# Kernel optimization log

Hardware: AMD Instinct MI355X
Metric: run time of the kernel (lower is better)

Reference implementation:

```python
import jax, jax.numpy as jnp
import numpy as np

NU = 3
NUM_MEM_TOKENS = 128
EPS = 1e-5


def dpfp(x, nu=NU):
    # x: [..., d] -> [..., 2*nu*d]; all outputs are >= 0
    x = jnp.concatenate([jax.nn.relu(x), jax.nn.relu(-x)], axis=-1)
    x_rolled = jnp.concatenate([jnp.roll(x, shift=j, axis=-1) for j in range(1, nu + 1)], axis=-1)
    x_repeat = jnp.concatenate([x] * nu, axis=-1)
    return x_repeat * x_rolled


def setup_inputs() -> dict:
    key = jax.random.key(0)
    ks = jax.random.split(key, 8)
    B, S, D, DM = 1, 16384, 2048, 64
    DK = 2 * NU * DM  # 384
    scale = 0.02
    return {
        "hidden_states": jax.random.normal(ks[0], (B, S, D), jnp.float32),
        "Wmq": jax.random.normal(ks[1], (DM, D), jnp.float32) * scale,
        "Wmk": jax.random.normal(ks[2], (DM, D), jnp.float32) * scale,
        "Wmv": jax.random.normal(ks[3], (D, D), jnp.float32) * scale,
        "Wmb_w": jax.random.normal(ks[4], (1, D), jnp.float32) * scale,
        "Wmb_b": jax.random.normal(ks[5], (1,), jnp.float32),
        "W_mem": jax.random.normal(ks[6], (B, DK, D), jnp.float32) * scale,
        "z": jax.random.uniform(ks[7], (B, DK), jnp.float32) + 0.1,
    }


def reference(hidden_states, Wmq, Wmk, Wmv, Wmb_w, Wmb_b, W_mem, z):
    # ---- associate (read from fast-weight memory) ----
    mq = dpfp(hidden_states @ Wmq.T)                       # [b,s,dk]
    num = jnp.einsum('ijk,ikt->ijt', mq, W_mem)            # [b,s,d]
    denom = jnp.einsum('ik,ijk->ij', z, mq)[..., None] + EPS
    hidden_states = num / denom + hidden_states

    # wrapped transformer layer modeled as identity
    out = hidden_states

    # ---- update_mem (write: recurrent outer-product accumulation) ----
    mem_tokens = out[:, -NUM_MEM_TOKENS:]                  # [b,m,d]
    mk = dpfp(mem_tokens @ Wmk.T)                          # [b,m,dk]
    new_mv = mem_tokens @ Wmv.T                            # [b,m,d]

    num2 = jnp.einsum('ijk,ikt->ijt', mk, W_mem)           # [b,m,d]
    denom2 = jnp.einsum('ij,ikj->ik', z, mk)[..., None] + EPS
    prev_mv = num2 / denom2

    mk_sq = jnp.sum(mk * mk, axis=-1)                      # ||mk||^2, [b,m]
    new_info_coef = 1.0 - denom2 / (mk_sq + EPS)[..., None]
    new_info_coef = jax.lax.stop_gradient(jnp.clip(new_info_coef, 0.0, 1.0))

    mv = new_mv - prev_mv
    mb = jax.nn.sigmoid(mem_tokens @ Wmb_w.T + Wmb_b)[..., 0]  # [b,m]
    associations = jnp.einsum('ijk,ijt,ij->ikt', mk, mv, mb)   # [b,dk,d]

    W_mem_new = W_mem + associations
    z_new = z + jnp.sum(new_info_coef * mk, axis=1)
    return out, W_mem_new, z_new
```

## Files before the change

### kernel.cpp

```cpp
#include <hip/hip_runtime.h>
#include <hip/hip_bf16.h>
#include <math.h>

#define S_ 16384
#define D_ 2048
#define DM_ 64
#define DK_ 384
#define NMEM_ 128
#define EPS_ 1e-5f

typedef __attribute__((ext_vector_type(8))) short bf16x8;
typedef __attribute__((ext_vector_type(8))) short s16x8;
typedef __attribute__((ext_vector_type(4))) float f32x4;
typedef unsigned short u16;

static __device__ __forceinline__ u16 f2bf(float x) {
    __hip_bfloat16 h = __float2bfloat16(x);
    return *reinterpret_cast<u16*>(&h);
}

static __device__ __forceinline__ void gload16(const void* g, void* l) {
    __builtin_amdgcn_global_load_lds(
        (const __attribute__((address_space(1))) unsigned int*)g,
        (__attribute__((address_space(3))) unsigned int*)l, 16, 0, 0);
}

__global__ __launch_bounds__(256) void k_prep(const float* __restrict__ Wmq,
                                              const float* __restrict__ Wmv,
                                              const float* __restrict__ Wmem,
                                              u16* __restrict__ Wmq_b,
                                              u16* __restrict__ Wmv_b,
                                              u16* __restrict__ WmT) {
    __shared__ float ts[32][33];
    const int bid = blockIdx.x;
    const int tid = threadIdx.x;
    if (bid < 4096) {
        size_t idx = ((size_t)bid * 256 + tid) * 4;
        float4 v = *reinterpret_cast<const float4*>(&Wmv[idx]);
        ushort4 p;
        p.x = f2bf(v.x); p.y = f2bf(v.y); p.z = f2bf(v.z); p.w = f2bf(v.w);
        *reinterpret_cast<ushort4*>(&Wmv_b[idx]) = p;
    } else if (bid < 4224) {
        int idx = ((bid - 4096) * 256 + tid) * 4;
        float4 v = *reinterpret_cast<const float4*>(&Wmq[idx]);
        ushort4 p;
        p.x = f2bf(v.x); p.y = f2bf(v.y); p.z = f2bf(v.z); p.w = f2bf(v.w);
        *reinterpret_cast<ushort4*>(&Wmq_b[idx]) = p;
    } else {
        int t = bid - 4224;
        int c0 = (t & 63) * 32, k0 = (t >> 6) * 32;
        const int tx = tid & 31, ty = tid >> 5;
#pragma unroll
        for (int i = 0; i < 4; ++i)
            ts[ty + 8 * i][tx] = Wmem[(size_t)(k0 + ty + 8 * i) * D_ + c0 + tx];
        __syncthreads();
#pragma unroll
        for (int i = 0; i < 4; ++i)
            WmT[(size_t)(c0 + ty + 8 * i) * DK_ + k0 + tx] = f2bf(ts[tx][ty + 8 * i]);
    }
}

__global__ __launch_bounds__(256) void k_qdp(const float* __restrict__ hs,
                                             const u16* __restrict__ Wmq_b,
                                             const float* __restrict__ z,
                                             u16* __restrict__ mq_b,
                                             float* __restrict__ denomv) {
    __shared__ u16 As[32 * 64];
    __shared__ u16 Bs[64 * 64];
    __shared__ float xs[32][128];
    __shared__ float zs[DK_];
    const int r0 = blockIdx.x * 32;
    const int tid = threadIdx.x;
    const int lane = tid & 63, w = tid >> 6;
    const int lrow = lane & 15, lkg = lane >> 4;
    const int wr = w >> 1, wc = w & 1;
    for (int i = tid; i < DK_; i += 256) zs[i] = z[i];
    f32x4 acc[2];
    const f32x4 zero4 = {0.f, 0.f, 0.f, 0.f};
    acc[0] = zero4; acc[1] = zero4;
    for (int kc = 0; kc < D_ / 64; ++kc) {
#pragma unroll
        for (int i = 0; i < 2; ++i) {
            int flat4 = tid + 256 * i;
            int row = flat4 >> 4, c4 = flat4 & 15;
            const float4 v = *reinterpret_cast<const float4*>(
                &hs[(size_t)(r0 + row) * D_ + kc * 64 + c4 * 4]);
            int off = row * 64 + (((c4 >> 1) ^ (row & 7)) * 8) + (c4 & 1) * 4;
            ushort4 p;
            p.x = f2bf(v.x); p.y = f2bf(v.y); p.z = f2bf(v.z); p.w = f2bf(v.w);
            *reinterpret_cast<ushort4*>(&As[off]) = p;
        }
#pragma unroll
        for (int i = 0; i < 2; ++i) {
            int col = w * 16 + i * 8 + (lane >> 3);
            int gg = (lane & 7) ^ (col & 7);
            gload16(Wmq_b + (size_t)col * D_ + kc * 64 + gg * 8,
                    &Bs[(w * 16 + i * 8) * 64]);
        }
        __syncthreads();
#pragma unroll
        for (int s = 0; s < 2; ++s) {
            int rl = wr * 16 + lrow;
            bf16x8 a_ = *reinterpret_cast<const bf16x8*>(
                &As[rl * 64 + (((s * 4 + lkg) ^ (rl & 7)) * 8)]);
#pragma unroll
            for (int n = 0; n < 2; ++n) {
                int cl = wc * 32 + n * 16 + lrow;
                bf16x8 b_ = *reinterpret_cast<const bf16x8*>(
                    &Bs[cl * 64 + (((s * 4 + lkg) ^ (cl & 7)) * 8)]);
                acc[n] = __builtin_amdgcn_mfma_f32_16x16x32_bf16(a_, b_, acc[n], 0, 0, 0);
            }
        }
        __syncthreads();
    }
#pragma unroll
    for (int n = 0; n < 2; ++n) {
        int col = wc * 32 + n * 16 + lrow;
#pragma unroll
        for (int r = 0; r < 4; ++r) {
            int row = wr * 16 + lkg * 4 + r;
            float q = acc[n][r];
            xs[row][col] = fmaxf(q, 0.f);
            xs[row][col + 64] = fmaxf(-q, 0.f);
        }
    }
    __syncthreads();
    {
        int row = tid >> 3, sub = tid & 7;
        float pd = 0.f;
#pragma unroll
        for (int c = 0; c < 6; ++c) {
            int base = sub * 48 + c * 8;
            int g = base >> 7;
            s16x8 pk;
#pragma unroll
            for (int e = 0; e < 8; ++e) {
                int m = base + e;
                int i = m & 127;
                float v = xs[row][i] * xs[row][(i - g - 1) & 127];
                pd += zs[m] * v;
                pk[e] = (short)f2bf(v);
            }
            *reinterpret_cast<s16x8*>(&mq_b[(size_t)(r0 + row) * DK_ + base]) = pk;
        }
        pd += __shfl_down(pd, 4, 8);
        pd += __shfl_down(pd, 2, 8);
        pd += __shfl_down(pd, 1, 8);
        if (sub == 0) denomv[r0 + row] = pd + EPS_;
    }
}

__global__ __launch_bounds__(256) void k_main(const float* __restrict__ hs,
                                              const u16* __restrict__ mq_b,
                                              const u16* __restrict__ WmT,
                                              const float* __restrict__ denomv,
                                              float* __restrict__ out) {
    __shared__ u16 At[128 * 64];
    __shared__ u16 Bt[128 * 64];
    __shared__ float dinv[128];
    const int bid = blockIdx.x;
    const int swz = (bid & 7) * 256 + (bid >> 3);
    const int r0 = (swz >> 4) * 128, c0 = (swz & 15) * 128;
    const int tid = threadIdx.x;
    const int lane = tid & 63, w = tid >> 6;
    const int lrow = lane & 15, lkg = lane >> 4;
    const int wr = w >> 1, wc = w & 1;
    if (tid < 128) dinv[tid] = 1.f / denomv[r0 + tid];
    f32x4 acc[4][4];
    const f32x4 zero4 = {0.f, 0.f, 0.f, 0.f};
#pragma unroll
    for (int m = 0; m < 4; ++m)
#pragma unroll
        for (int n = 0; n < 4; ++n) acc[m][n] = zero4;
    for (int kc = 0; kc < 6; ++kc) {
#pragma unroll
        for (int i = 0; i < 4; ++i) {
            int rr = w * 32 + i * 8 + (lane >> 3);
            int gg = (lane & 7) ^ (rr & 7);
            gload16(mq_b + (size_t)(r0 + rr) * DK_ + kc * 64 + gg * 8,
                    &At[(w * 32 + i * 8) * 64]);
            gload16(WmT + (size_t)(c0 + rr) * DK_ + kc * 64 + gg * 8,
                    &Bt[(w * 32 + i * 8) * 64]);
        }
        __syncthreads();
#pragma unroll
        for (int s = 0; s < 2; ++s) {
            bf16x8 af[4], bb[4];
#pragma unroll
            for (int m = 0; m < 4; ++m) {
                int rl = wr * 64 + m * 16 + lrow;
                af[m] = *reinterpret_cast<const bf16x8*>(
                    &At[rl * 64 + (((s * 4 + lkg) ^ (rl & 7)) * 8)]);
            }
#pragma unroll
            for (int n = 0; n < 4; ++n) {
                int cl = wc * 64 + n * 16 + lrow;
                bb[n] = *reinterpret_cast<const bf16x8*>(
                    &Bt[cl * 64 + (((s * 4 + lkg) ^ (cl & 7)) * 8)]);
            }
#pragma unroll
            for (int m = 0; m < 4; ++m)
#pragma unroll
                for (int n = 0; n < 4; ++n)
                    acc[m][n] = __builtin_amdgcn_mfma_f32_16x16x32_bf16(
                        af[m], bb[n], acc[m][n], 0, 0, 0);
        }
        __syncthreads();
    }
#pragma unroll
    for (int m = 0; m < 4; ++m)
#pragma unroll
        for (int n = 0; n < 4; ++n) {
            int colg = c0 + wc * 64 + n * 16 + lrow;
#pragma unroll
            for (int r = 0; r < 4; ++r) {
                int rowl = wr * 64 + m * 16 + lkg * 4 + r;
                size_t off = (size_t)(r0 + rowl) * D_ + colg;
                out[off] = acc[m][n][r] * dinv[rowl] + hs[off];
            }
        }
}

__global__ __launch_bounds__(256) void k_mk(const float* __restrict__ out,
                                            const float* __restrict__ Wmk,
                                            const float* __restrict__ Wmb_w,
                                            const float* __restrict__ Wmb_b,
                                            const float* __restrict__ z,
                                            float* __restrict__ mk_g,
                                            u16* __restrict__ mk_b,
                                            u16* __restrict__ mem_b,
                                            float* __restrict__ scal) {
    __shared__ float memRow[D_];
    __shared__ float qpart[4][64];
    __shared__ float xv[128];
    __shared__ float mks[DK_];
    __shared__ float red[256];
    const int j = blockIdx.x;
    const int tid = threadIdx.x;
    const float* mem = out + (size_t)(S_ - NMEM_ + j) * D_;
    const float4* mem4 = reinterpret_cast<const float4*>(mem);
    float4* mr4 = reinterpret_cast<float4*>(memRow);
#pragma unroll
    for (int i4 = tid; i4 < 512; i4 += 256) {
        float4 v = mem4[i4];
        mr4[i4] = v;
        ushort4 p;
        p.x = f2bf(v.x); p.y = f2bf(v.y); p.z = f2bf(v.z); p.w = f2bf(v.w);
        *reinterpret_cast<ushort4*>(&mem_b[(size_t)j * D_ + i4 * 4]) = p;
    }
    __syncthreads();
    {
        int c = tid & 63, seg = tid >> 6;
        const float4* wrow = reinterpret_cast<const float4*>(Wmk + (size_t)c * D_);
        float p = 0.f;
#pragma unroll 4
        for (int k4 = seg * 128; k4 < seg * 128 + 128; ++k4) {
            float4 a = mr4[k4], b = wrow[k4];
            p += a.x * b.x + a.y * b.y + a.z * b.z + a.w * b.w;
        }
        qpart[seg][c] = p;
    }
    __syncthreads();
    if (tid < 64) {
        float q = qpart[0][tid] + qpart[1][tid] + qpart[2][tid] + qpart[3][tid];
        xv[tid] = fmaxf(q, 0.f);
        xv[tid + 64] = fmaxf(-q, 0.f);
    }
    __syncthreads();
    for (int m = tid; m < DK_; m += 256) {
        int i = m & 127, g = m >> 7;
        float v = xv[i] * xv[(i - g - 1) & 127];
        mks[m] = v;
        mk_g[(size_t)j * DK_ + m] = v;
        mk_b[(size_t)j * DK_ + m] = f2bf(v);
    }
    __syncthreads();
    float pd = 0.f, ps = 0.f;
    for (int m = tid; m < DK_; m += 256) { float v = mks[m]; pd += v * z[m]; ps += v * v; }
    red[tid] = pd; __syncthreads();
    for (int s = 128; s > 0; s >>= 1) { if (tid < s) red[tid] += red[tid + s]; __syncthreads(); }
    float denom2 = red[0] + EPS_;
    __syncthreads();
    red[tid] = ps; __syncthreads();
    for (int s = 128; s > 0; s >>= 1) { if (tid < s) red[tid] += red[tid + s]; __syncthreads(); }
    float mksq = red[0];
    __syncthreads();
    float pb = 0.f;
    {
        const float4* wb4 = reinterpret_cast<const float4*>(Wmb_w);
#pragma unroll
        for (int k4 = tid; k4 < 512; k4 += 256) {
            float4 a = mr4[k4], b = wb4[k4];
            pb += a.x * b.x + a.y * b.y + a.z * b.z + a.w * b.w;
        }
    }
    red[tid] = pb; __syncthreads();
    for (int s = 128; s > 0; s >>= 1) { if (tid < s) red[tid] += red[tid + s]; __syncthreads(); }
    if (tid == 0) {
        float bsum = red[0] + Wmb_b[0];
        float mb = 1.f / (1.f + expf(-bsum));
        float nic = 1.f - denom2 / (mksq + EPS_);
        nic = fminf(fmaxf(nic, 0.f), 1.f);
        scal[j * 4 + 0] = denom2;
        scal[j * 4 + 1] = nic;
        scal[j * 4 + 2] = mb;
        scal[j * 4 + 3] = mksq;
    }
}

__global__ __launch_bounds__(256) void k_mv(const u16* __restrict__ mem_b,
                                            const u16* __restrict__ Wmv_b,
                                            const u16* __restrict__ mk_b,
                                            const u16* __restrict__ WmT,
                                            const float* __restrict__ scal,
                                            float* __restrict__ mvb) {
    __shared__ u16 At[128 * 64];
    __shared__ u16 Bt[64 * 64];
    __shared__ float inv2[128];
    __shared__ float mbl[128];
    const int c0 = blockIdx.x * 64;
    const int tid = threadIdx.x;
    const int lane = tid & 63, w = tid >> 6;
    const int lrow = lane & 15, lkg = lane >> 4;
    const int wr = w >> 1, wc = w & 1;
    if (tid < 128) {
        inv2[tid] = 1.f / scal[tid * 4 + 0];
        mbl[tid] = scal[tid * 4 + 2];
    }
    f32x4 acc1[4][2], acc2[4][2];
    const f32x4 zero4 = {0.f, 0.f, 0.f, 0.f};
#pragma unroll
    for (int m = 0; m < 4; ++m)
#pragma unroll
        for (int n = 0; n < 2; ++n) { acc1[m][n] = zero4; acc2[m][n] = zero4; }
    for (int kc = 0; kc < D_ / 64; ++kc) {
#pragma unroll
        for (int i = 0; i < 4; ++i) {
            int rr = w * 32 + i * 8 + (lane >> 3);
            int gg = (lane & 7) ^ (rr & 7);
            gload16(mem_b + (size_t)rr * D_ + kc * 64 + gg * 8,
                    &At[(w * 32 + i * 8) * 64]);
        }
#pragma unroll
        for (int i = 0; i < 2; ++i) {
            int cc = w * 16 + i * 8 + (lane >> 3);
            int gg = (lane & 7) ^ (cc & 7);
            gload16(Wmv_b + (size_t)(c0 + cc) * D_ + kc * 64 + gg * 8,
                    &Bt[(w * 16 + i * 8) * 64]);
        }
        __syncthreads();
#pragma unroll
        for (int s = 0; s < 2; ++s) {
            bf16x8 af[4], bb[2];
#pragma unroll
            for (int m = 0; m < 4; ++m) {
                int rl = wr * 64 + m * 16 + lrow;
                af[m] = *reinterpret_cast<const bf16x8*>(
                    &At[rl * 64 + (((s * 4 + lkg) ^ (rl & 7)) * 8)]);
            }
#pragma unroll
            for (int n = 0; n < 2; ++n) {
                int cl = wc * 32 + n * 16 + lrow;
                bb[n] = *reinterpret_cast<const bf16x8*>(
                    &Bt[cl * 64 + (((s * 4 + lkg) ^ (cl & 7)) * 8)]);
            }
#pragma unroll
            for (int m = 0; m < 4; ++m)
#pragma unroll
                for (int n = 0; n < 2; ++n)
                    acc1[m][n] = __builtin_amdgcn_mfma_f32_16x16x32_bf16(
                        af[m], bb[n], acc1[m][n], 0, 0, 0);
        }
        __syncthreads();
    }
    for (int kc = 0; kc < 6; ++kc) {
#pragma unroll
        for (int i = 0; i < 4; ++i) {
            int rr = w * 32 + i * 8 + (lane >> 3);
            int gg = (lane & 7) ^ (rr & 7);
            gload16(mk_b + (size_t)rr * DK_ + kc * 64 + gg * 8,
                    &At[(w * 32 + i * 8) * 64]);
        }
#pragma unroll
        for (int i = 0; i < 2; ++i) {
            int cc = w * 16 + i * 8 + (lane >> 3);
            int gg = (lane & 7) ^ (cc & 7);
            gload16(WmT + (size_t)(c0 + cc) * DK_ + kc * 64 + gg * 8,
                    &Bt[(w * 16 + i * 8) * 64]);
        }
        __syncthreads();
#pragma unroll
        for (int s = 0; s < 2; ++s) {
            bf16x8 af[4], bb[2];
#pragma unroll
            for (int m = 0; m < 4; ++m) {
                int rl = wr * 64 + m * 16 + lrow;
                af[m] = *reinterpret_cast<const bf16x8*>(
                    &At[rl * 64 + (((s * 4 + lkg) ^ (rl & 7)) * 8)]);
            }
#pragma unroll
            for (int n = 0; n < 2; ++n) {
                int cl = wc * 32 + n * 16 + lrow;
                bb[n] = *reinterpret_cast<const bf16x8*>(
                    &Bt[cl * 64 + (((s * 4 + lkg) ^ (cl & 7)) * 8)]);
            }
#pragma unroll
            for (int m = 0; m < 4; ++m)
#pragma unroll
                for (int n = 0; n < 2; ++n)
                    acc2[m][n] = __builtin_amdgcn_mfma_f32_16x16x32_bf16(
                        af[m], bb[n], acc2[m][n], 0, 0, 0);
        }
        __syncthreads();
    }
#pragma unroll
    for (int m = 0; m < 4; ++m)
#pragma unroll
        for (int n = 0; n < 2; ++n) {
            int colg = c0 + wc * 32 + n * 16 + lrow;
#pragma unroll
            for (int r = 0; r < 4; ++r) {
                int j = wr * 64 + m * 16 + lkg * 4 + r;
                mvb[(size_t)j * D_ + colg] =
                    (acc1[m][n][r] - acc2[m][n][r] * inv2[j]) * mbl[j];
            }
        }
}

__global__ __launch_bounds__(256) void k_wmem(const float* __restrict__ Wmem,
                                              const float* __restrict__ mk_g,
                                              const float* __restrict__ mvb,
                                              const float* __restrict__ scal,
                                              const float* __restrict__ z,
                                              float* __restrict__ wout,
                                              float* __restrict__ zout) {
    const int tid = threadIdx.x;
    if (blockIdx.y == 48) {
        if (blockIdx.x == 0) {
            for (int t = tid; t < DK_; t += 256) {
                float acc = z[t];
                for (int j = 0; j < NMEM_; ++j)
                    acc += scal[j * 4 + 1] * mk_g[(size_t)j * DK_ + t];
                zout[t] = acc;
            }
        }
        return;
    }
    const int c0 = blockIdx.x * 256;
    const int k0 = blockIdx.y * 8;
    const int tk = tid >> 5, tt = tid & 31;
    const float4* mvb4 = reinterpret_cast<const float4*>(mvb);
    f32x4 acc[2] = {{0.f, 0.f, 0.f, 0.f}, {0.f, 0.f, 0.f, 0.f}};
#pragma unroll 4
    for (int j = 0; j < NMEM_; ++j) {
        float a = mk_g[(size_t)j * DK_ + k0 + tk];
#pragma unroll
        for (int i = 0; i < 2; ++i) {
            float4 v = mvb4[((size_t)j * D_ + c0 + tt * 4 + 128 * i) >> 2];
            acc[i][0] += a * v.x; acc[i][1] += a * v.y;
            acc[i][2] += a * v.z; acc[i][3] += a * v.w;
        }
    }
#pragma unroll
    for (int i = 0; i < 2; ++i) {
        size_t off = (size_t)(k0 + tk) * D_ + c0 + tt * 4 + 128 * i;
        float4 wv = *reinterpret_cast<const float4*>(&Wmem[off]);
        float4 o;
        o.x = wv.x + acc[i][0]; o.y = wv.y + acc[i][1];
        o.z = wv.z + acc[i][2]; o.w = wv.w + acc[i][3];
        *reinterpret_cast<float4*>(&wout[off]) = o;
    }
}

extern "C" void kernel_launch(void* const* d_in, const int* in_sizes, int n_in,
                              void* d_out, int out_size, void* d_ws, size_t ws_size,
                              hipStream_t stream) {
    const float* hs   = (const float*)d_in[0];
    const float* Wmq  = (const float*)d_in[1];
    const float* Wmk  = (const float*)d_in[2];
    const float* Wmv  = (const float*)d_in[3];
    const float* Wmbw = (const float*)d_in[4];
    const float* Wmbb = (const float*)d_in[5];
    const float* Wmem = (const float*)d_in[6];
    const float* z    = (const float*)d_in[7];
    float* out  = (float*)d_out;
    float* wout = out + (size_t)S_ * D_;
    float* zout = wout + (size_t)DK_ * D_;

    float* ws = (float*)d_ws;
    float* denomv = ws;
    float* mk_g   = denomv + S_;
    float* scal   = mk_g + (size_t)NMEM_ * DK_;
    float* mvb    = scal + NMEM_ * 4;
    u16* mq_b  = (u16*)(mvb + (size_t)NMEM_ * D_);
    u16* WmT   = mq_b + (size_t)S_ * DK_;
    u16* Wmq_b = WmT + (size_t)D_ * DK_;
    u16* Wmv_b = Wmq_b + (size_t)DM_ * D_;
    u16* mem_b = Wmv_b + (size_t)D_ * D_;
    u16* mk_b  = mem_b + (size_t)NMEM_ * D_;

    k_prep<<<dim3(4992), 256, 0, stream>>>(Wmq, Wmv, Wmem, Wmq_b, Wmv_b, WmT);
    k_qdp<<<dim3(S_ / 32), 256, 0, stream>>>(hs, Wmq_b, z, mq_b, denomv);
    k_main<<<dim3((S_ / 128) * (D_ / 128)), 256, 0, stream>>>(hs, mq_b, WmT, denomv, out);
    k_mk<<<dim3(NMEM_), 256, 0, stream>>>(out, Wmk, Wmbw, Wmbb, z, mk_g, mk_b, mem_b, scal);
    k_mv<<<dim3(D_ / 64), 256, 0, stream>>>(mem_b, Wmv_b, mk_b, WmT, scal, mvb);
    k_wmem<<<dim3(D_ / 256, DK_ / 8 + 1), 256, 0, stream>>>(Wmem, mk_g, mvb, scal, z, wout, zout);
}
```

Measured before the change: 198.2 us.

## Fuse DPFP query projection with memory readout GEMM in one kernel

Merges k_qdp and k_main into a single kernel. Each 32-row block computes the query projection, builds the DPFP features as bf16 A-fragments held in registers, then sweeps all 2048 output columns against WmT staged in shared memory. This removes the global round trip of mq_b and denomv and one launch. The cost is a much smaller row tile (32 rows instead of 128), so WmT (about 1.5 MB in bf16) is reloaded by each of 512 blocks. The DPFP inputs are also now rounded to bf16 before the products are taken.

```diff
diff --git a/kernel.cpp b/kernel.cpp
--- a/kernel.cpp
+++ b/kernel.cpp
@@ -17,6 +17,11 @@
 static __device__ __forceinline__ u16 f2bf(float x) {
     __hip_bfloat16 h = __float2bfloat16(x);
     return *reinterpret_cast<u16*>(&h);
+}
+
+static __device__ __forceinline__ float bf2f(u16 u) {
+    union { unsigned int i; float f; } c; c.i = ((unsigned int)u) << 16;
+    return c.f;
 }
 
 static __device__ __forceinline__ void gload16(const void* g, void* l) {
@@ -60,24 +65,26 @@
     }
 }
 
-__global__ __launch_bounds__(256) void k_qdp(const float* __restrict__ hs,
-                                             const u16* __restrict__ Wmq_b,
-                                             const float* __restrict__ z,
-                                             u16* __restrict__ mq_b,
-                                             float* __restrict__ denomv) {
-    __shared__ u16 As[32 * 64];
-    __shared__ u16 Bs[64 * 64];
-    __shared__ float xs[32][128];
+__global__ __launch_bounds__(256) void k_fuse(const float* __restrict__ hs,
+                                              const u16* __restrict__ Wmq_b,
+                                              const u16* __restrict__ WmT,
+                                              const float* __restrict__ z,
+                                              float* __restrict__ out) {
+    __shared__ u16 sbuf[16384];
     __shared__ float zs[DK_];
+    __shared__ float dinvS[32];
     const int r0 = blockIdx.x * 32;
     const int tid = threadIdx.x;
     const int lane = tid & 63, w = tid >> 6;
     const int lrow = lane & 15, lkg = lane >> 4;
     const int wr = w >> 1, wc = w & 1;
     for (int i = tid; i < DK_; i += 256) zs[i] = z[i];
-    f32x4 acc[2];
+
+    u16* As = sbuf;
+    u16* Bs = sbuf + 2048;
+    f32x4 q1[2];
     const f32x4 zero4 = {0.f, 0.f, 0.f, 0.f};
-    acc[0] = zero4; acc[1] = zero4;
+    q1[0] = zero4; q1[1] = zero4;
     for (int kc = 0; kc < D_ / 64; ++kc) {
 #pragma unroll
         for (int i = 0; i < 2; ++i) {
@@ -108,117 +115,90 @@
                 int cl = wc * 32 + n * 16 + lrow;
                 bf16x8 b_ = *reinterpret_cast<const bf16x8*>(
                     &Bs[cl * 64 + (((s * 4 + lkg) ^ (cl & 7)) * 8)]);
-                acc[n] = __builtin_amdgcn_mfma_f32_16x16x32_bf16(a_, b_, acc[n], 0, 0, 0);
-            }
-        }
-        __syncthreads();
-    }
+                q1[n] = __builtin_amdgcn_mfma_f32_16x16x32_bf16(a_, b_, q1[n], 0, 0, 0);
+            }
+        }
+        __syncthreads();
+    }
+
+    u16* xs = sbuf;
 #pragma unroll
     for (int n = 0; n < 2; ++n) {
         int col = wc * 32 + n * 16 + lrow;
 #pragma unroll
         for (int r = 0; r < 4; ++r) {
             int row = wr * 16 + lkg * 4 + r;
-            float q = acc[n][r];
-            xs[row][col] = fmaxf(q, 0.f);
-            xs[row][col + 64] = fmaxf(-q, 0.f);
-        }
-    }
-    __syncthreads();
+            float qv = q1[n][r];
+            xs[row * 136 + col] = f2bf(fmaxf(qv, 0.f));
+            xs[row * 136 + col + 64] = f2bf(fmaxf(-qv, 0.f));
+        }
+    }
+    __syncthreads();
+
+    bf16x8 af[12];
+    float pd = 0.f;
     {
-        int row = tid >> 3, sub = tid & 7;
-        float pd = 0.f;
-#pragma unroll
-        for (int c = 0; c < 6; ++c) {
-            int base = sub * 48 + c * 8;
-            int g = base >> 7;
-            s16x8 pk;
+        int arow = wr * 16 + lrow;
+#pragma unroll
+        for (int f = 0; f < 12; ++f) {
+            bf16x8 pk;
 #pragma unroll
             for (int e = 0; e < 8; ++e) {
-                int m = base + e;
-                int i = m & 127;
-                float v = xs[row][i] * xs[row][(i - g - 1) & 127];
+                int m = f * 32 + lkg * 8 + e;
+                int g = m >> 7, i = m & 127;
+                float v = bf2f(xs[arow * 136 + i]) *
+                          bf2f(xs[arow * 136 + ((i - g - 1) & 127)]);
                 pd += zs[m] * v;
                 pk[e] = (short)f2bf(v);
             }
-            *reinterpret_cast<s16x8*>(&mq_b[(size_t)(r0 + row) * DK_ + base]) = pk;
-        }
-        pd += __shfl_down(pd, 4, 8);
-        pd += __shfl_down(pd, 2, 8);
-        pd += __shfl_down(pd, 1, 8);
-        if (sub == 0) denomv[r0 + row] = pd + EPS_;
-    }
-}
-
-__global__ __launch_bounds__(256) void k_main(const float* __restrict__ hs,
-                                              const u16* __restrict__ mq_b,
-                                              const u16* __restrict__ WmT,
-                                              const float* __restrict__ denomv,
-                                              float* __restrict__ out) {
-    __shared__ u16 At[128 * 64];
-    __shared__ u16 Bt[128 * 64];
-    __shared__ float dinv[128];
-    const int bid = blockIdx.x;
-    const int swz = (bid & 7) * 256 + (bid >> 3);
-    const int r0 = (swz >> 4) * 128, c0 = (swz & 15) * 128;
-    const int tid = threadIdx.x;
-    const int lane = tid & 63, w = tid >> 6;
-    const int lrow = lane & 15, lkg = lane >> 4;
-    const int wr = w >> 1, wc = w & 1;
-    if (tid < 128) dinv[tid] = 1.f / denomv[r0 + tid];
-    f32x4 acc[4][4];
-    const f32x4 zero4 = {0.f, 0.f, 0.f, 0.f};
-#pragma unroll
-    for (int m = 0; m < 4; ++m)
-#pragma unroll
-        for (int n = 0; n < 4; ++n) acc[m][n] = zero4;
-    for (int kc = 0; kc < 6; ++kc) {
-#pragma unroll
-        for (int i = 0; i < 4; ++i) {
-            int rr = w * 32 + i * 8 + (lane >> 3);
-            int gg = (lane & 7) ^ (rr & 7);
-            gload16(mq_b + (size_t)(r0 + rr) * DK_ + kc * 64 + gg * 8,
-                    &At[(w * 32 + i * 8) * 64]);
-            gload16(WmT + (size_t)(c0 + rr) * DK_ + kc * 64 + gg * 8,
-                    &Bt[(w * 32 + i * 8) * 64]);
-        }
-        __syncthreads();
-#pragma unroll
-        for (int s = 0; s < 2; ++s) {
-            bf16x8 af[4], bb[4];
-#pragma unroll
-            for (int m = 0; m < 4; ++m) {
-                int rl = wr * 64 + m * 16 + lrow;
-                af[m] = *reinterpret_cast<const bf16x8*>(
-                    &At[rl * 64 + (((s * 4 + lkg) ^ (rl & 7)) * 8)]);
-            }
-#pragma unroll
-            for (int n = 0; n < 4; ++n) {
-                int cl = wc * 64 + n * 16 + lrow;
-                bb[n] = *reinterpret_cast<const bf16x8*>(
-                    &Bt[cl * 64 + (((s * 4 + lkg) ^ (cl & 7)) * 8)]);
-            }
-#pragma unroll
-            for (int m = 0; m < 4; ++m)
-#pragma unroll
-                for (int n = 0; n < 4; ++n)
-                    acc[m][n] = __builtin_amdgcn_mfma_f32_16x16x32_bf16(
-                        af[m], bb[n], acc[m][n], 0, 0, 0);
-        }
-        __syncthreads();
-    }
-#pragma unroll
-    for (int m = 0; m < 4; ++m)
+            af[f] = pk;
+        }
+        pd += __shfl_xor(pd, 16);
+        pd += __shfl_xor(pd, 32);
+        if (wc == 0 && lane < 16) dinvS[wr * 16 + lane] = 1.f / (pd + EPS_);
+    }
+    __syncthreads();
+
+    f32x4 acc[4];
+#pragma unroll
+    for (int n = 0; n < 4; ++n) acc[n] = zero4;
+    for (int ct = 0; ct < 16; ++ct) {
+        const int c0 = ct * 128;
+        for (int kc = 0; kc < 3; ++kc) {
+#pragma unroll
+            for (int i = 0; i < 8; ++i) {
+                int flat = w * 64 + (lane) + 256 * i;
+                int cc = flat >> 4, g4 = flat & 15;
+                int gswz = g4 ^ (cc & 7);
+                gload16(WmT + (size_t)(c0 + cc) * DK_ + kc * 128 + gswz * 8,
+                        &sbuf[(w * 64 + 256 * i) * 8]);
+            }
+            __syncthreads();
+#pragma unroll
+            for (int s = 0; s < 4; ++s) {
+#pragma unroll
+                for (int n = 0; n < 4; ++n) {
+                    int cl = wc * 64 + n * 16 + lrow;
+                    bf16x8 bb = *reinterpret_cast<const bf16x8*>(
+                        &sbuf[cl * 128 + (((s * 4 + lkg) ^ (cl & 7)) * 8)]);
+                    acc[n] = __builtin_amdgcn_mfma_f32_16x16x32_bf16(
+                        af[kc * 4 + s], bb, acc[n], 0, 0, 0);
+                }
+            }
+            __syncthreads();
+        }
 #pragma unroll
         for (int n = 0; n < 4; ++n) {
             int colg = c0 + wc * 64 + n * 16 + lrow;
 #pragma unroll
             for (int r = 0; r < 4; ++r) {
-                int rowl = wr * 64 + m * 16 + lkg * 4 + r;
+                int rowl = wr * 16 + lkg * 4 + r;
                 size_t off = (size_t)(r0 + rowl) * D_ + colg;
-                out[off] = acc[m][n][r] * dinv[rowl] + hs[off];
-            }
-        }
+                out[off] = acc[n][r] * dinvS[rowl] + hs[off];
+            }
+            acc[n] = zero4;
+        }
+    }
 }
 
 __global__ __launch_bounds__(256) void k_mk(const float* __restrict__ out,
@@ -488,20 +468,17 @@
     float* zout = wout + (size_t)DK_ * D_;
 
     float* ws = (float*)d_ws;
-    float* denomv = ws;
-    float* mk_g   = denomv + S_;
+    float* mk_g   = ws;
     float* scal   = mk_g + (size_t)NMEM_ * DK_;
     float* mvb    = scal + NMEM_ * 4;
-    u16* mq_b  = (u16*)(mvb + (size_t)NMEM_ * D_);
-    u16* WmT   = mq_b + (size_t)S_ * DK_;
+    u16* WmT   = (u16*)(mvb + (size_t)NMEM_ * D_);
     u16* Wmq_b = WmT + (size_t)D_ * DK_;
     u16* Wmv_b = Wmq_b + (size_t)DM_ * D_;
     u16* mem_b = Wmv_b + (size_t)D_ * D_;
     u16* mk_b  = mem_b + (size_t)NMEM_ * D_;
 
     k_prep<<<dim3(4992), 256, 0, stream>>>(Wmq, Wmv, Wmem, Wmq_b, Wmv_b, WmT);
-    k_qdp<<<dim3(S_ / 32), 256, 0, stream>>>(hs, Wmq_b, z, mq_b, denomv);
-    k_main<<<dim3((S_ / 128) * (D_ / 128)), 256, 0, stream>>>(hs, mq_b, WmT, denomv, out);
+    k_fuse<<<dim3(S_ / 32), 256, 0, stream>>>(hs, Wmq_b, WmT, z, out);
     k_mk<<<dim3(NMEM_), 256, 0, stream>>>(out, Wmk, Wmbw, Wmbb, z, mk_g, mk_b, mem_b, scal);
     k_mv<<<dim3(D_ / 64), 256, 0, stream>>>(mem_b, Wmv_b, mk_b, WmT, scal, mvb);
     k_wmem<<<dim3(D_ / 256, DK_ / 8 + 1), 256, 0, stream>>>(Wmem, mk_g, mvb, scal, z, wout, zout);
```

Measured after the change: 236.2 us. +19.1%, slower.

## Double-buffer k_qdp K-loop and stage k_main epilogue through LDS for coalesced stores

Applied to the files above, without the earlier changes.

k_qdp now double-buffers its A and B tiles, issuing the next chunk's global loads before the MFMAs on the current chunk and converting and storing them afterwards. This drops one barrier per iteration and overlaps load latency with compute. k_main's epilogue now stages the scaled accumulator through LDS in two 64-row halves, then does coalesced float4 reads of hs and float4 writes of out. This replaces the scattered scalar stores, at the cost of extra LDS traffic and barriers.

```diff
diff --git a/kernel.cpp b/kernel.cpp
--- a/kernel.cpp
+++ b/kernel.cpp
@@ -65,10 +65,9 @@
                                              const float* __restrict__ z,
                                              u16* __restrict__ mq_b,
                                              float* __restrict__ denomv) {
-    __shared__ u16 As[32 * 64];
-    __shared__ u16 Bs[64 * 64];
-    __shared__ float xs[32][128];
+    __shared__ __align__(16) u16 qbuf[12288];
     __shared__ float zs[DK_];
+    float* xs = reinterpret_cast<float*>(qbuf);
     const int r0 = blockIdx.x * 32;
     const int tid = threadIdx.x;
     const int lane = tid & 63, w = tid >> 6;
@@ -78,40 +77,70 @@
     f32x4 acc[2];
     const f32x4 zero4 = {0.f, 0.f, 0.f, 0.f};
     acc[0] = zero4; acc[1] = zero4;
-    for (int kc = 0; kc < D_ / 64; ++kc) {
-#pragma unroll
-        for (int i = 0; i < 2; ++i) {
-            int flat4 = tid + 256 * i;
-            int row = flat4 >> 4, c4 = flat4 & 15;
-            const float4 v = *reinterpret_cast<const float4*>(
-                &hs[(size_t)(r0 + row) * D_ + kc * 64 + c4 * 4]);
-            int off = row * 64 + (((c4 >> 1) ^ (row & 7)) * 8) + (c4 & 1) * 4;
-            ushort4 p;
-            p.x = f2bf(v.x); p.y = f2bf(v.y); p.z = f2bf(v.z); p.w = f2bf(v.w);
-            *reinterpret_cast<ushort4*>(&As[off]) = p;
-        }
+    const int arow0 = tid >> 4, ac4_0 = tid & 15;
+    const int arow1 = (tid + 256) >> 4, ac4_1 = (tid + 256) & 15;
+    const int aoff0 = arow0 * 64 + (((ac4_0 >> 1) ^ (arow0 & 7)) * 8) + (ac4_0 & 1) * 4;
+    const int aoff1 = arow1 * 64 + (((ac4_1 >> 1) ^ (arow1 & 7)) * 8) + (ac4_1 & 1) * 4;
+    {
+        float4 v0 = *reinterpret_cast<const float4*>(&hs[(size_t)(r0 + arow0) * D_ + ac4_0 * 4]);
+        float4 v1 = *reinterpret_cast<const float4*>(&hs[(size_t)(r0 + arow1) * D_ + ac4_1 * 4]);
+        ushort4 p0, p1;
+        p0.x = f2bf(v0.x); p0.y = f2bf(v0.y); p0.z = f2bf(v0.z); p0.w = f2bf(v0.w);
+        p1.x = f2bf(v1.x); p1.y = f2bf(v1.y); p1.z = f2bf(v1.z); p1.w = f2bf(v1.w);
+        *reinterpret_cast<ushort4*>(&qbuf[aoff0]) = p0;
+        *reinterpret_cast<ushort4*>(&qbuf[aoff1]) = p1;
 #pragma unroll
         for (int i = 0; i < 2; ++i) {
             int col = w * 16 + i * 8 + (lane >> 3);
             int gg = (lane & 7) ^ (col & 7);
-            gload16(Wmq_b + (size_t)col * D_ + kc * 64 + gg * 8,
-                    &Bs[(w * 16 + i * 8) * 64]);
-        }
-        __syncthreads();
+            gload16(Wmq_b + (size_t)col * D_ + gg * 8, &qbuf[4096 + (w * 16 + i * 8) * 64]);
+        }
+    }
+    __syncthreads();
+    int cur = 0;
+    for (int kc = 0; kc < 32; ++kc) {
+        const int nxt = cur ^ 1;
+        const bool hasN = (kc + 1) < 32;
+        u16* Acur = qbuf + cur * 2048;
+        u16* Anxt = qbuf + nxt * 2048;
+        u16* Bcur = qbuf + 4096 + cur * 4096;
+        u16* Bnxt = qbuf + 4096 + nxt * 4096;
+        float4 v0, v1;
+        if (hasN) {
+            v0 = *reinterpret_cast<const float4*>(
+                &hs[(size_t)(r0 + arow0) * D_ + (kc + 1) * 64 + ac4_0 * 4]);
+            v1 = *reinterpret_cast<const float4*>(
+                &hs[(size_t)(r0 + arow1) * D_ + (kc + 1) * 64 + ac4_1 * 4]);
+#pragma unroll
+            for (int i = 0; i < 2; ++i) {
+                int col = w * 16 + i * 8 + (lane >> 3);
+                int gg = (lane & 7) ^ (col & 7);
+                gload16(Wmq_b + (size_t)col * D_ + (kc + 1) * 64 + gg * 8,
+                        &Bnxt[(w * 16 + i * 8) * 64]);
+            }
+        }
 #pragma unroll
         for (int s = 0; s < 2; ++s) {
             int rl = wr * 16 + lrow;
             bf16x8 a_ = *reinterpret_cast<const bf16x8*>(
-                &As[rl * 64 + (((s * 4 + lkg) ^ (rl & 7)) * 8)]);
+                &Acur[rl * 64 + (((s * 4 + lkg) ^ (rl & 7)) * 8)]);
 #pragma unroll
             for (int n = 0; n < 2; ++n) {
                 int cl = wc * 32 + n * 16 + lrow;
                 bf16x8 b_ = *reinterpret_cast<const bf16x8*>(
-                    &Bs[cl * 64 + (((s * 4 + lkg) ^ (cl & 7)) * 8)]);
+                    &Bcur[cl * 64 + (((s * 4 + lkg) ^ (cl & 7)) * 8)]);
                 acc[n] = __builtin_amdgcn_mfma_f32_16x16x32_bf16(a_, b_, acc[n], 0, 0, 0);
             }
         }
-        __syncthreads();
+        if (hasN) {
+            ushort4 p0, p1;
+            p0.x = f2bf(v0.x); p0.y = f2bf(v0.y); p0.z = f2bf(v0.z); p0.w = f2bf(v0.w);
+            p1.x = f2bf(v1.x); p1.y = f2bf(v1.y); p1.z = f2bf(v1.z); p1.w = f2bf(v1.w);
+            *reinterpret_cast<ushort4*>(&Anxt[aoff0]) = p0;
+            *reinterpret_cast<ushort4*>(&Anxt[aoff1]) = p1;
+        }
+        __syncthreads();
+        cur ^= 1;
     }
 #pragma unroll
     for (int n = 0; n < 2; ++n) {
@@ -120,8 +149,8 @@
         for (int r = 0; r < 4; ++r) {
             int row = wr * 16 + lkg * 4 + r;
             float q = acc[n][r];
-            xs[row][col] = fmaxf(q, 0.f);
-            xs[row][col + 64] = fmaxf(-q, 0.f);
+            xs[row * 128 + col] = fmaxf(q, 0.f);
+            xs[row * 128 + col + 64] = fmaxf(-q, 0.f);
         }
     }
     __syncthreads();
@@ -137,7 +166,7 @@
             for (int e = 0; e < 8; ++e) {
                 int m = base + e;
                 int i = m & 127;
-                float v = xs[row][i] * xs[row][(i - g - 1) & 127];
+                float v = xs[row * 128 + i] * xs[row * 128 + ((i - g - 1) & 127)];
                 pd += zs[m] * v;
                 pk[e] = (short)f2bf(v);
             }
@@ -155,9 +184,10 @@
                                               const u16* __restrict__ WmT,
                                               const float* __restrict__ denomv,
                                               float* __restrict__ out) {
-    __shared__ u16 At[128 * 64];
-    __shared__ u16 Bt[128 * 64];
+    __shared__ __align__(16) u16 ldsbuf[16384];
     __shared__ float dinv[128];
+    u16* At = ldsbuf;
+    u16* Bt = ldsbuf + 8192;
     const int bid = blockIdx.x;
     const int swz = (bid & 7) * 256 + (bid >> 3);
     const int r0 = (swz >> 4) * 128, c0 = (swz & 15) * 128;
@@ -207,18 +237,36 @@
         }
         __syncthreads();
     }
-#pragma unroll
-    for (int m = 0; m < 4; ++m)
-#pragma unroll
-        for (int n = 0; n < 4; ++n) {
-            int colg = c0 + wc * 64 + n * 16 + lrow;
-#pragma unroll
-            for (int r = 0; r < 4; ++r) {
-                int rowl = wr * 64 + m * 16 + lkg * 4 + r;
-                size_t off = (size_t)(r0 + rowl) * D_ + colg;
-                out[off] = acc[m][n][r] * dinv[rowl] + hs[off];
-            }
-        }
+    float* ldsf = reinterpret_cast<float*>(ldsbuf);
+    float4* ldsf4 = reinterpret_cast<float4*>(ldsbuf);
+#pragma unroll
+    for (int h = 0; h < 2; ++h) {
+        if (wr == h) {
+#pragma unroll
+            for (int m = 0; m < 4; ++m)
+#pragma unroll
+                for (int n = 0; n < 4; ++n) {
+                    int col = wc * 64 + n * 16 + lrow;
+#pragma unroll
+                    for (int r = 0; r < 4; ++r) {
+                        int rowl = m * 16 + lkg * 4 + r;
+                        ldsf[rowl * 128 + col] = acc[m][n][r] * dinv[h * 64 + rowl];
+                    }
+                }
+        }
+        __syncthreads();
+#pragma unroll
+        for (int i = 0; i < 8; ++i) {
+            int idx4 = tid + 256 * i;
+            int rowl = idx4 >> 5, c4 = idx4 & 31;
+            float4 v = ldsf4[idx4];
+            size_t off = (size_t)(r0 + h * 64 + rowl) * D_ + c0 + c4 * 4;
+            const float4 hv = *reinterpret_cast<const float4*>(&hs[off]);
+            v.x += hv.x; v.y += hv.y; v.z += hv.z; v.w += hv.w;
+            *reinterpret_cast<float4*>(&out[off]) = v;
+        }
+        __syncthreads();
+    }
 }
 
 __global__ __launch_bounds__(256) void k_mk(const float* __restrict__ out,
```

Result: no change. 202.1 us (+2.0%).

## Fuse bf16 conversion of Wmv/mem into k_mv, retile k_qdp, coalesce k_main epilogue

Applied to the files above, without the earlier changes.

Drops the separate fp32-to-bf16 conversion of Wmv (a 2048x2048 matrix) and of the memory tokens. k_mv now reads fp32 directly and converts while staging into LDS, which removes a large prep write/read pass. k_qdp moves to 16-row tiles with one MFMA per wave, doubling the block count for better occupancy and sharing one LDS buffer between phases. k_main's epilogue is staged through LDS so the output stores and hs reads become coalesced float4 accesses, at the cost of extra barriers.

```diff
diff --git a/kernel.cpp b/kernel.cpp
--- a/kernel.cpp
+++ b/kernel.cpp
@@ -26,28 +26,20 @@
 }
 
 __global__ __launch_bounds__(256) void k_prep(const float* __restrict__ Wmq,
-                                              const float* __restrict__ Wmv,
                                               const float* __restrict__ Wmem,
                                               u16* __restrict__ Wmq_b,
-                                              u16* __restrict__ Wmv_b,
                                               u16* __restrict__ WmT) {
     __shared__ float ts[32][33];
     const int bid = blockIdx.x;
     const int tid = threadIdx.x;
-    if (bid < 4096) {
-        size_t idx = ((size_t)bid * 256 + tid) * 4;
-        float4 v = *reinterpret_cast<const float4*>(&Wmv[idx]);
-        ushort4 p;
-        p.x = f2bf(v.x); p.y = f2bf(v.y); p.z = f2bf(v.z); p.w = f2bf(v.w);
-        *reinterpret_cast<ushort4*>(&Wmv_b[idx]) = p;
-    } else if (bid < 4224) {
-        int idx = ((bid - 4096) * 256 + tid) * 4;
+    if (bid < 128) {
+        int idx = (bid * 256 + tid) * 4;
         float4 v = *reinterpret_cast<const float4*>(&Wmq[idx]);
         ushort4 p;
         p.x = f2bf(v.x); p.y = f2bf(v.y); p.z = f2bf(v.z); p.w = f2bf(v.w);
         *reinterpret_cast<ushort4*>(&Wmq_b[idx]) = p;
     } else {
-        int t = bid - 4224;
+        int t = bid - 128;
         int c0 = (t & 63) * 32, k0 = (t >> 6) * 32;
         const int tx = tid & 31, ty = tid >> 5;
 #pragma unroll
@@ -65,30 +57,26 @@
                                              const float* __restrict__ z,
                                              u16* __restrict__ mq_b,
                                              float* __restrict__ denomv) {
-    __shared__ u16 As[32 * 64];
-    __shared__ u16 Bs[64 * 64];
-    __shared__ float xs[32][128];
+    __shared__ __align__(16) u16 qbuf[5376];
     __shared__ float zs[DK_];
-    const int r0 = blockIdx.x * 32;
+    u16* As = qbuf;
+    u16* Bs = qbuf + 1024;
+    float* xs = reinterpret_cast<float*>(qbuf);
+    const int r0 = blockIdx.x * 16;
     const int tid = threadIdx.x;
     const int lane = tid & 63, w = tid >> 6;
     const int lrow = lane & 15, lkg = lane >> 4;
-    const int wr = w >> 1, wc = w & 1;
     for (int i = tid; i < DK_; i += 256) zs[i] = z[i];
-    f32x4 acc[2];
-    const f32x4 zero4 = {0.f, 0.f, 0.f, 0.f};
-    acc[0] = zero4; acc[1] = zero4;
-    for (int kc = 0; kc < D_ / 64; ++kc) {
-#pragma unroll
-        for (int i = 0; i < 2; ++i) {
-            int flat4 = tid + 256 * i;
-            int row = flat4 >> 4, c4 = flat4 & 15;
+    f32x4 acc = {0.f, 0.f, 0.f, 0.f};
+    const int arow = tid >> 4, ac4 = tid & 15;
+    const int aoff = arow * 64 + (((ac4 >> 1) ^ (arow & 7)) * 8) + (ac4 & 1) * 4;
+    for (int kc = 0; kc < 32; ++kc) {
+        {
             const float4 v = *reinterpret_cast<const float4*>(
-                &hs[(size_t)(r0 + row) * D_ + kc * 64 + c4 * 4]);
-            int off = row * 64 + (((c4 >> 1) ^ (row & 7)) * 8) + (c4 & 1) * 4;
+                &hs[(size_t)(r0 + arow) * D_ + kc * 64 + ac4 * 4]);
             ushort4 p;
             p.x = f2bf(v.x); p.y = f2bf(v.y); p.z = f2bf(v.z); p.w = f2bf(v.w);
-            *reinterpret_cast<ushort4*>(&As[off]) = p;
+            *reinterpret_cast<ushort4*>(&As[aoff]) = p;
         }
 #pragma unroll
         for (int i = 0; i < 2; ++i) {
@@ -100,52 +88,48 @@
         __syncthreads();
 #pragma unroll
         for (int s = 0; s < 2; ++s) {
-            int rl = wr * 16 + lrow;
             bf16x8 a_ = *reinterpret_cast<const bf16x8*>(
-                &As[rl * 64 + (((s * 4 + lkg) ^ (rl & 7)) * 8)]);
-#pragma unroll
-            for (int n = 0; n < 2; ++n) {
-                int cl = wc * 32 + n * 16 + lrow;
-                bf16x8 b_ = *reinterpret_cast<const bf16x8*>(
-                    &Bs[cl * 64 + (((s * 4 + lkg) ^ (cl & 7)) * 8)]);
-                acc[n] = __builtin_amdgcn_mfma_f32_16x16x32_bf16(a_, b_, acc[n], 0, 0, 0);
-            }
-        }
-        __syncthreads();
-    }
-#pragma unroll
-    for (int n = 0; n < 2; ++n) {
-        int col = wc * 32 + n * 16 + lrow;
+                &As[lrow * 64 + (((s * 4 + lkg) ^ (lrow & 7)) * 8)]);
+            int cl = w * 16 + lrow;
+            bf16x8 b_ = *reinterpret_cast<const bf16x8*>(
+                &Bs[cl * 64 + (((s * 4 + lkg) ^ (cl & 7)) * 8)]);
+            acc = __builtin_amdgcn_mfma_f32_16x16x32_bf16(a_, b_, acc, 0, 0, 0);
+        }
+        __syncthreads();
+    }
+    {
+        int col = w * 16 + lrow;
 #pragma unroll
         for (int r = 0; r < 4; ++r) {
-            int row = wr * 16 + lkg * 4 + r;
-            float q = acc[n][r];
-            xs[row][col] = fmaxf(q, 0.f);
-            xs[row][col + 64] = fmaxf(-q, 0.f);
+            int row = lkg * 4 + r;
+            float q = acc[r];
+            xs[row * 132 + col] = fmaxf(q, 0.f);
+            xs[row * 132 + col + 64] = fmaxf(-q, 0.f);
         }
     }
     __syncthreads();
     {
-        int row = tid >> 3, sub = tid & 7;
+        int row = tid >> 4, sub = tid & 15;
         float pd = 0.f;
 #pragma unroll
-        for (int c = 0; c < 6; ++c) {
-            int base = sub * 48 + c * 8;
+        for (int c = 0; c < 3; ++c) {
+            int base = sub * 24 + c * 8;
             int g = base >> 7;
             s16x8 pk;
 #pragma unroll
             for (int e = 0; e < 8; ++e) {
                 int m = base + e;
                 int i = m & 127;
-                float v = xs[row][i] * xs[row][(i - g - 1) & 127];
+                float v = xs[row * 132 + i] * xs[row * 132 + ((i - g - 1) & 127)];
                 pd += zs[m] * v;
                 pk[e] = (short)f2bf(v);
             }
             *reinterpret_cast<s16x8*>(&mq_b[(size_t)(r0 + row) * DK_ + base]) = pk;
         }
-        pd += __shfl_down(pd, 4, 8);
-        pd += __shfl_down(pd, 2, 8);
-        pd += __shfl_down(pd, 1, 8);
+        pd += __shfl_down(pd, 8, 16);
+        pd += __shfl_down(pd, 4, 16);
+        pd += __shfl_down(pd, 2, 16);
+        pd += __shfl_down(pd, 1, 16);
         if (sub == 0) denomv[r0 + row] = pd + EPS_;
     }
 }
@@ -155,9 +139,10 @@
                                               const u16* __restrict__ WmT,
                                               const float* __restrict__ denomv,
                                               float* __restrict__ out) {
-    __shared__ u16 At[128 * 64];
-    __shared__ u16 Bt[128 * 64];
+    __shared__ __align__(16) u16 ldsbuf[16384];
     __shared__ float dinv[128];
+    u16* At = ldsbuf;
+    u16* Bt = ldsbuf + 8192;
     const int bid = blockIdx.x;
     const int swz = (bid & 7) * 256 + (bid >> 3);
     const int r0 = (swz >> 4) * 128, c0 = (swz & 15) * 128;
@@ -207,18 +192,36 @@
         }
         __syncthreads();
     }
-#pragma unroll
-    for (int m = 0; m < 4; ++m)
-#pragma unroll
-        for (int n = 0; n < 4; ++n) {
-            int colg = c0 + wc * 64 + n * 16 + lrow;
-#pragma unroll
-            for (int r = 0; r < 4; ++r) {
-                int rowl = wr * 64 + m * 16 + lkg * 4 + r;
-                size_t off = (size_t)(r0 + rowl) * D_ + colg;
-                out[off] = acc[m][n][r] * dinv[rowl] + hs[off];
-            }
-        }
+    float* ldsf = reinterpret_cast<float*>(ldsbuf);
+    float4* ldsf4 = reinterpret_cast<float4*>(ldsbuf);
+#pragma unroll
+    for (int h = 0; h < 2; ++h) {
+        if (wr == h) {
+#pragma unroll
+            for (int m = 0; m < 4; ++m)
+#pragma unroll
+                for (int n = 0; n < 4; ++n) {
+                    int col = wc * 64 + n * 16 + lrow;
+#pragma unroll
+                    for (int r = 0; r < 4; ++r) {
+                        int rowl = m * 16 + lkg * 4 + r;
+                        ldsf[rowl * 128 + col] = acc[m][n][r] * dinv[h * 64 + rowl];
+                    }
+                }
+        }
+        __syncthreads();
+#pragma unroll
+        for (int i = 0; i < 8; ++i) {
+            int idx4 = tid + 256 * i;
+            int rowl = idx4 >> 5, c4 = idx4 & 31;
+            float4 v = ldsf4[idx4];
+            size_t off = (size_t)(r0 + h * 64 + rowl) * D_ + c0 + c4 * 4;
+            const float4 hv = *reinterpret_cast<const float4*>(&hs[off]);
+            v.x += hv.x; v.y += hv.y; v.z += hv.z; v.w += hv.w;
+            *reinterpret_cast<float4*>(&out[off]) = v;
+        }
+        __syncthreads();
+    }
 }
 
 __global__ __launch_bounds__(256) void k_mk(const float* __restrict__ out,
@@ -228,7 +231,6 @@
                                             const float* __restrict__ z,
                                             float* __restrict__ mk_g,
                                             u16* __restrict__ mk_b,
-                                            u16* __restrict__ mem_b,
                                             float* __restrict__ scal) {
     __shared__ float memRow[D_];
     __shared__ float qpart[4][64];
@@ -241,13 +243,7 @@
     const float4* mem4 = reinterpret_cast<const float4*>(mem);
     float4* mr4 = reinterpret_cast<float4*>(memRow);
 #pragma unroll
-    for (int i4 = tid; i4 < 512; i4 += 256) {
-        float4 v = mem4[i4];
-        mr4[i4] = v;
-        ushort4 p;
-        p.x = f2bf(v.x); p.y = f2bf(v.y); p.z = f2bf(v.z); p.w = f2bf(v.w);
-        *reinterpret_cast<ushort4*>(&mem_b[(size_t)j * D_ + i4 * 4]) = p;
-    }
+    for (int i4 = tid; i4 < 512; i4 += 256) mr4[i4] = mem4[i4];
     __syncthreads();
     {
         int c = tid & 63, seg = tid >> 6;
@@ -308,8 +304,8 @@
     }
 }
 
-__global__ __launch_bounds__(256) void k_mv(const u16* __restrict__ mem_b,
-                                            const u16* __restrict__ Wmv_b,
+__global__ __launch_bounds__(256) void k_mv(const float* __restrict__ out,
+                                            const float* __restrict__ Wmv,
                                             const u16* __restrict__ mk_b,
                                             const u16* __restrict__ WmT,
                                             const float* __restrict__ scal,
@@ -327,6 +323,7 @@
         inv2[tid] = 1.f / scal[tid * 4 + 0];
         mbl[tid] = scal[tid * 4 + 2];
     }
+    const float* memp = out + (size_t)(S_ - NMEM_) * D_;
     f32x4 acc1[4][2], acc2[4][2];
     const f32x4 zero4 = {0.f, 0.f, 0.f, 0.f};
 #pragma unroll
@@ -335,18 +332,26 @@
         for (int n = 0; n < 2; ++n) { acc1[m][n] = zero4; acc2[m][n] = zero4; }
     for (int kc = 0; kc < D_ / 64; ++kc) {
 #pragma unroll
+        for (int i = 0; i < 8; ++i) {
+            int flat4 = tid + 256 * i;
+            int row = flat4 >> 4, c4 = flat4 & 15;
+            const float4 v = *reinterpret_cast<const float4*>(
+                &memp[(size_t)row * D_ + kc * 64 + c4 * 4]);
+            int off = row * 64 + (((c4 >> 1) ^ (row & 7)) * 8) + (c4 & 1) * 4;
+            ushort4 p;
+            p.x = f2bf(v.x); p.y = f2bf(v.y); p.z = f2bf(v.z); p.w = f2bf(v.w);
+            *reinterpret_cast<ushort4*>(&At[off]) = p;
+        }
+#pragma unroll
         for (int i = 0; i < 4; ++i) {
-            int rr = w * 32 + i * 8 + (lane >> 3);
-            int gg = (lane & 7) ^ (rr & 7);
-            gload16(mem_b + (size_t)rr * D_ + kc * 64 + gg * 8,
-                    &At[(w * 32 + i * 8) * 64]);
-        }
-#pragma unroll
-        for (int i = 0; i < 2; ++i) {
-            int cc = w * 16 + i * 8 + (lane >> 3);
-            int gg = (lane & 7) ^ (cc & 7);
-            gload16(Wmv_b + (size_t)(c0 + cc) * D_ + kc * 64 + gg * 8,
-                    &Bt[(w * 16 + i * 8) * 64]);
+            int flat4 = tid + 256 * i;
+            int row = flat4 >> 4, c4 = flat4 & 15;
+            const float4 v = *reinterpret_cast<const float4*>(
+                &Wmv[(size_t)(c0 + row) * D_ + kc * 64 + c4 * 4]);
+            int off = row * 64 + (((c4 >> 1) ^ (row & 7)) * 8) + (c4 & 1) * 4;
+            ushort4 p;
+            p.x = f2bf(v.x); p.y = f2bf(v.y); p.z = f2bf(v.z); p.w = f2bf(v.w);
+            *reinterpret_cast<ushort4*>(&Bt[off]) = p;
         }
         __syncthreads();
 #pragma unroll
@@ -495,14 +500,12 @@
     u16* mq_b  = (u16*)(mvb + (size_t)NMEM_ * D_);
     u16* WmT   = mq_b + (size_t)S_ * DK_;
     u16* Wmq_b = WmT + (size_t)D_ * DK_;
-    u16* Wmv_b = Wmq_b + (size_t)DM_ * D_;
-    u16* mem_b = Wmv_b + (size_t)D_ * D_;
-    u16* mk_b  = mem_b + (size_t)NMEM_ * D_;
-
-    k_prep<<<dim3(4992), 256, 0, stream>>>(Wmq, Wmv, Wmem, Wmq_b, Wmv_b, WmT);
-    k_qdp<<<dim3(S_ / 32), 256, 0, stream>>>(hs, Wmq_b, z, mq_b, denomv);
+    u16* mk_b  = Wmq_b + (size_t)DM_ * D_;
+
+    k_prep<<<dim3(896), 256, 0, stream>>>(Wmq, Wmem, Wmq_b, WmT);
+    k_qdp<<<dim3(S_ / 16), 256, 0, stream>>>(hs, Wmq_b, z, mq_b, denomv);
     k_main<<<dim3((S_ / 128) * (D_ / 128)), 256, 0, stream>>>(hs, mq_b, WmT, denomv, out);
-    k_mk<<<dim3(NMEM_), 256, 0, stream>>>(out, Wmk, Wmbw, Wmbb, z, mk_g, mk_b, mem_b, scal);
-    k_mv<<<dim3(D_ / 64), 256, 0, stream>>>(mem_b, Wmv_b, mk_b, WmT, scal, mvb);
+    k_mk<<<dim3(NMEM_), 256, 0, stream>>>(out, Wmk, Wmbw, Wmbb, z, mk_g, mk_b, scal);
+    k_mv<<<dim3(D_ / 64), 256, 0, stream>>>(out, Wmv, mk_b, WmT, scal, mvb);
     k_wmem<<<dim3(D_ / 256, DK_ / 8 + 1), 256, 0, stream>>>(Wmem, mk_g, mvb, scal, z, wout, zout);
 }
```

New measurement: 202.6 us. 2.2% more time.
